# Performance work log

Measured on AMD Instinct MI355X. Metric: run time of the kernel, lower is better.

## Reference

```python
import jax, jax.numpy as jnp
import numpy as np
import math

RCR = 5.2
NUM_SPECIES = 7
AEV_DIM = 1008
WIDTHS = [1008, 256, 192, 160]


def setup_inputs() -> dict:
    key = jax.random.key(0)
    ks = jax.random.split(key, 12)
    B, N = 1, 2048
    species = jax.random.randint(ks[0], (B, N), 0, NUM_SPECIES, dtype=jnp.int64 if jax.config.read('jax_enable_x64') else jnp.int32)
    coordinates = jax.random.uniform(ks[1], (B, N, 3), dtype=jnp.float32) * 6.0
    EtaR = jnp.array([16.0], dtype=jnp.float32)
    ShfR = jnp.array([0.9 + 0.18 * x for x in range(16)], dtype=jnp.float32)
    s = 0.05
    W0 = jax.random.normal(ks[2], (NUM_SPECIES, WIDTHS[1], WIDTHS[0]), jnp.float32) * s
    b0 = jax.random.normal(ks[3], (NUM_SPECIES, WIDTHS[1]), jnp.float32) * s
    W1 = jax.random.normal(ks[4], (NUM_SPECIES, WIDTHS[2], WIDTHS[1]), jnp.float32) * s
    b1 = jax.random.normal(ks[5], (NUM_SPECIES, WIDTHS[2]), jnp.float32) * s
    W2 = jax.random.normal(ks[6], (NUM_SPECIES, WIDTHS[3], WIDTHS[2]), jnp.float32) * s
    b2 = jax.random.normal(ks[7], (NUM_SPECIES, WIDTHS[3]), jnp.float32) * s
    Wf = jax.random.normal(ks[8], (NUM_SPECIES, 1, WIDTHS[3]), jnp.float32) * s
    bf = jax.random.normal(ks[9], (NUM_SPECIES, 1), jnp.float32) * s
    return {'species': species, 'coordinates': coordinates, 'EtaR': EtaR, 'ShfR': ShfR,
            'W0': W0, 'b0': b0, 'W1': W1, 'b1': b1, 'W2': W2, 'b2': b2, 'Wf': Wf, 'bf': bf}


def _celu(x, alpha=0.1):
    return jnp.maximum(x, 0.0) + jnp.minimum(0.0, alpha * jnp.expm1(x / alpha))


def _aev(species, coordinates, EtaR, ShfR):
    B, N = species.shape
    diff = coordinates[:, :, None, :] - coordinates[:, None, :, :]  # [B,N,N,3]
    dsq = jnp.sum(diff * diff, axis=-1)
    safe = jnp.where(dsq > 0, dsq, 1.0)
    dist = jnp.sqrt(safe)  # [B,N,N], diag is a dummy 1.0
    mask = (dsq > 0) & (dist <= RCR)
    fc = (0.5 * jnp.cos(math.pi * dist / RCR) + 0.5) * mask.astype(jnp.float32)
    onehot = jax.nn.one_hot(species, NUM_SPECIES, dtype=jnp.float32)  # [B,N,S]
    core = jnp.exp(-EtaR[0] * (dist[..., None] - ShfR) ** 2)  # [B,N,N,R]
    weighted = core * fc[..., None]
    # sum over neighbor j, grouped by neighbor species s (species-major concat order)
    radial = jnp.einsum('bijr,bjs->bisr', weighted, onehot)  # [B,N,S,R]
    radial = radial.reshape(B, N, NUM_SPECIES * ShfR.shape[0])
    pad = AEV_DIM - radial.shape[-1]
    return jnp.pad(radial, ((0, 0), (0, 0), (0, pad)))


def reference(species, coordinates, EtaR, ShfR, W0, b0, W1, b1, W2, b2, Wf, bf):
    aev = _aev(species, coordinates, EtaR, ShfR)  # [B,N,1008]
    # run all 7 element nets on every atom (matches the module's redundant-compute semantics)
    h = _celu(jnp.einsum('soh,bnh->sbno', W0, aev) + b0[:, None, None, :])
    h = _celu(jnp.einsum('soh,sbnh->sbno', W1, h) + b1[:, None, None, :])
    h = _celu(jnp.einsum('soh,sbnh->sbno', W2, h) + b2[:, None, None, :])
    e = jnp.einsum('soh,sbnh->sbno', Wf, h) + bf[:, None, None, :]  # [S,B,N,1]
    onehot = jax.nn.one_hot(species, NUM_SPECIES, dtype=jnp.float32)  # [B,N,S]
    total = jnp.einsum('sbn,bns->', e[..., 0], onehot)
    return total.reshape(1)
```

## Files before the change

kernel.cpp:

```cpp
#include <hip/hip_runtime.h>

#define N_ATOMS 2048
#define NSPEC 7
#define NR 16
#define NFEAT 112
#define K0P 128
#define RCR_F 5.2f
#define H0 256
#define H1 192
#define H2 160
#define W0_PITCH 1008
#define NTILE16 128
#define GY2 (H2 / 16)
#define NPART (NSPEC * GY2 * NTILE16)

typedef __attribute__((ext_vector_type(8))) short short8;
typedef __attribute__((ext_vector_type(4))) float floatx4;

#define WS_SEG     0
#define WS_SCOORD  16384
#define WS_AEVB    65536
#define WS_H0B     655360
#define WS_H1B     1769472
#define WS_WB0     2621440
#define WS_WB1     3145728
#define WS_WB2     3866624
#define WS_PART    4325376

__device__ __forceinline__ float celu01(float x) {
    return x > 0.f ? x : 0.1f * (__expf(x * 10.f) - 1.f);
}

__device__ __forceinline__ unsigned short f2bf(float x) {
    unsigned int u = __float_as_uint(x);
    u = (u + 0x7FFFu + ((u >> 16) & 1u)) >> 16;
    return (unsigned short)u;
}

__global__ __launch_bounds__(256) void sort_kernel(const int* __restrict__ species,
                                                   const float* __restrict__ coords,
                                                   int* __restrict__ seg,
                                                   float4* __restrict__ scoord,
                                                   float* __restrict__ out) {
    __shared__ int cnt[NSPEC];
    __shared__ int cur[NSPEC];
    int t = threadIdx.x;
    if (t < NSPEC) cnt[t] = 0;
    __syncthreads();
    for (int a = t; a < N_ATOMS; a += 256) atomicAdd(&cnt[species[a]], 1);
    __syncthreads();
    if (t == 0) {
        int run = 0;
        for (int s = 0; s < NSPEC; s++) { seg[s] = run; cur[s] = run; run += cnt[s]; }
        seg[NSPEC] = run;
        out[0] = 0.0f;
    }
    __syncthreads();
    for (int a = t; a < N_ATOMS; a += 256) {
        int sp = species[a];
        int pos = atomicAdd(&cur[sp], 1);
        scoord[pos] = make_float4(coords[3*a], coords[3*a+1], coords[3*a+2], 0.f);
    }
}

#define S0E (NSPEC * H0 * K0P)
#define S1E (NSPEC * H1 * H0)
#define S2E (NSPEC * H2 * H1)
__global__ __launch_bounds__(256) void prep_kernel(const float* __restrict__ W0,
                                                   const float* __restrict__ W1,
                                                   const float* __restrict__ W2,
                                                   unsigned short* __restrict__ wb0,
                                                   unsigned short* __restrict__ wb1,
                                                   unsigned short* __restrict__ wb2) {
    int idx = blockIdx.x * 256 + threadIdx.x;
    if (idx < S0E) {
        int k = idx & 127, r = idx >> 7;
        float v = (k < NFEAT) ? W0[(size_t)r * W0_PITCH + k] : 0.f;
        wb0[idx] = f2bf(v);
    } else if (idx < S0E + S1E) {
        int j = idx - S0E;
        wb1[j] = f2bf(W1[j]);
    } else if (idx < S0E + S1E + S2E) {
        int j = idx - S0E - S1E;
        wb2[j] = f2bf(W2[j]);
    }
}

__global__ __launch_bounds__(256) void aev_kernel(const float4* __restrict__ scoord,
                                                  const int* __restrict__ seg,
                                                  const float* __restrict__ ShfR,
                                                  const float* __restrict__ EtaR,
                                                  unsigned short* __restrict__ aevb) {
    int s = blockIdx.y;
    int p = blockIdx.x * 4 + (threadIdx.x >> 6);
    int lane = threadIdx.x & 63;

    float4 ci = scoord[p];
    float eta = EtaR[0];
    float shf[NR];
#pragma unroll
    for (int r = 0; r < NR; r++) shf[r] = ShfR[r];
    float acc[NR];
#pragma unroll
    for (int r = 0; r < NR; r++) acc[r] = 0.f;

    int kbeg = seg[s] + lane;
    int kend = seg[s + 1];
    const float rc2 = RCR_F * RCR_F;
    const float cosk = 3.14159265358979f / RCR_F;

    for (int k = kbeg; k < kend; k += 64) {
        float4 cj = scoord[k];
        float dx = ci.x - cj.x, dy = ci.y - cj.y, dz = ci.z - cj.z;
        float dsq = dx*dx + dy*dy + dz*dz;
        bool valid = (dsq > 0.f) && (dsq <= rc2);
        float d = sqrtf(dsq);
        float fc = 0.5f * __cosf(d * cosk) + 0.5f;
        fc = valid ? fc : 0.f;
#pragma unroll
        for (int r = 0; r < NR; r++) {
            float u = d - shf[r];
            acc[r] = fmaf(__expf(-eta * u * u), fc, acc[r]);
        }
    }
#pragma unroll
    for (int r = 0; r < NR; r++) {
        float v = acc[r];
        v += __shfl_xor(v, 1);
        v += __shfl_xor(v, 2);
        v += __shfl_xor(v, 4);
        v += __shfl_xor(v, 8);
        v += __shfl_xor(v, 16);
        v += __shfl_xor(v, 32);
        acc[r] = v;
    }
    if (lane == 0) {
        unsigned short* dst = aevb + (size_t)p * K0P + s * NR;
#pragma unroll
        for (int r = 0; r < NR; r++) dst[r] = f2bf(acc[r]);
        if (s == 0) {
            unsigned short* pz = aevb + (size_t)p * K0P + NFEAT;
#pragma unroll
            for (int r = 0; r < K0P - NFEAT; r++) pz[r] = 0;
        }
    }
}

template<int KSTEPS, int KP, int NTOT, int NPOUT>
__global__ __launch_bounds__(64) void mfma_layer(const unsigned short* __restrict__ act,
                                                 const unsigned short* __restrict__ wb,
                                                 const float* __restrict__ bias,
                                                 const int* __restrict__ seg,
                                                 unsigned short* __restrict__ outbuf) {
    int s = blockIdx.z;
    int segend = seg[s + 1];
    int base = seg[s] + blockIdx.x * 16;
    if (base >= segend) return;
    int nbase = blockIdx.y * 16;

    int lane = threadIdx.x;
    int r = lane & 15, quad = lane >> 4;

    const unsigned short* arow = act + (size_t)(base + r) * KP + quad * 8;
    const unsigned short* brow = wb + ((size_t)(s * NTOT + nbase + r)) * KP + quad * 8;

    floatx4 acc = {0.f, 0.f, 0.f, 0.f};
#pragma unroll
    for (int ks = 0; ks < KSTEPS; ks++) {
        short8 a = *(const short8*)(arow + ks * 32);
        short8 b = *(const short8*)(brow + ks * 32);
        acc = __builtin_amdgcn_mfma_f32_16x16x32_bf16(a, b, acc, 0, 0, 0);
    }
    float bi = bias[s * NTOT + nbase + r];
#pragma unroll
    for (int reg = 0; reg < 4; reg++) {
        int atom = base + quad * 4 + reg;
        if (atom < segend)
            outbuf[(size_t)atom * NPOUT + nbase + r] = f2bf(celu01(acc[reg] + bi));
    }
}

__global__ __launch_bounds__(64) void mfma_final(const unsigned short* __restrict__ act,
                                                 const unsigned short* __restrict__ wb,
                                                 const float* __restrict__ bias,
                                                 const float* __restrict__ Wf,
                                                 const int* __restrict__ seg,
                                                 float* __restrict__ part) {
    int s = blockIdx.z;
    int pidx = (s * GY2 + blockIdx.y) * NTILE16 + blockIdx.x;
    int segend = seg[s + 1];
    int base = seg[s] + blockIdx.x * 16;
    int lane = threadIdx.x;
    if (base >= segend) {
        if (lane == 0) part[pidx] = 0.f;
        return;
    }
    int nbase = blockIdx.y * 16;
    int r = lane & 15, quad = lane >> 4;

    const unsigned short* arow = act + (size_t)(base + r) * H1 + quad * 8;
    const unsigned short* brow = wb + ((size_t)(s * H2 + nbase + r)) * H1 + quad * 8;

    floatx4 acc = {0.f, 0.f, 0.f, 0.f};
#pragma unroll
    for (int ks = 0; ks < H1 / 32; ks++) {
        short8 a = *(const short8*)(arow + ks * 32);
        short8 b = *(const short8*)(brow + ks * 32);
        acc = __builtin_amdgcn_mfma_f32_16x16x32_bf16(a, b, acc, 0, 0, 0);
    }
    float bi = bias[s * H2 + nbase + r];
    float wf = Wf[s * H2 + nbase + r];
    float e = 0.f;
#pragma unroll
    for (int reg = 0; reg < 4; reg++) {
        int atom = base + quad * 4 + reg;
        if (atom < segend) e += wf * celu01(acc[reg] + bi);
    }
    e += __shfl_xor(e, 1);
    e += __shfl_xor(e, 2);
    e += __shfl_xor(e, 4);
    e += __shfl_xor(e, 8);
    e += __shfl_xor(e, 16);
    e += __shfl_xor(e, 32);
    if (lane == 0) part[pidx] = e;
}

__global__ __launch_bounds__(256) void reduce_kernel(const float* __restrict__ part,
                                                     const int* __restrict__ seg,
                                                     const float* __restrict__ bf,
                                                     float* __restrict__ out) {
    __shared__ float wsum[4];
    int t = threadIdx.x;
    float v = 0.f;
    for (int i = t; i < NPART; i += 256) v += part[i];
    v += __shfl_down(v, 32);
    v += __shfl_down(v, 16);
    v += __shfl_down(v, 8);
    v += __shfl_down(v, 4);
    v += __shfl_down(v, 2);
    v += __shfl_down(v, 1);
    if ((t & 63) == 0) wsum[t >> 6] = v;
    __syncthreads();
    if (t == 0) {
        float tot = wsum[0] + wsum[1] + wsum[2] + wsum[3];
        for (int s = 0; s < NSPEC; s++) tot += (float)(seg[s + 1] - seg[s]) * bf[s];
        out[0] = tot;
    }
}

extern "C" void kernel_launch(void* const* d_in, const int* in_sizes, int n_in,
                              void* d_out, int out_size, void* d_ws, size_t ws_size,
                              hipStream_t stream) {
    const int*   species = (const int*)d_in[0];
    const float* coords  = (const float*)d_in[1];
    const float* EtaR    = (const float*)d_in[2];
    const float* ShfR    = (const float*)d_in[3];
    const float* W0      = (const float*)d_in[4];
    const float* b0      = (const float*)d_in[5];
    const float* W1      = (const float*)d_in[6];
    const float* b1      = (const float*)d_in[7];
    const float* W2      = (const float*)d_in[8];
    const float* b2      = (const float*)d_in[9];
    const float* Wf      = (const float*)d_in[10];
    const float* bf      = (const float*)d_in[11];
    float* out = (float*)d_out;
    char* ws = (char*)d_ws;

    int*            seg    = (int*)(ws + WS_SEG);
    float4*         scoord = (float4*)(ws + WS_SCOORD);
    unsigned short* aevb   = (unsigned short*)(ws + WS_AEVB);
    unsigned short* h0b    = (unsigned short*)(ws + WS_H0B);
    unsigned short* h1b    = (unsigned short*)(ws + WS_H1B);
    unsigned short* wb0    = (unsigned short*)(ws + WS_WB0);
    unsigned short* wb1    = (unsigned short*)(ws + WS_WB1);
    unsigned short* wb2    = (unsigned short*)(ws + WS_WB2);
    float*          part   = (float*)(ws + WS_PART);

    hipLaunchKernelGGL(sort_kernel, dim3(1), dim3(256), 0, stream,
                       species, coords, seg, scoord, out);
    hipLaunchKernelGGL(prep_kernel, dim3((S0E + S1E + S2E + 255) / 256), dim3(256), 0, stream,
                       W0, W1, W2, wb0, wb1, wb2);
    hipLaunchKernelGGL(aev_kernel, dim3(N_ATOMS / 4, NSPEC), dim3(256), 0, stream,
                       scoord, seg, ShfR, EtaR, aevb);
    hipLaunchKernelGGL((mfma_layer<K0P / 32, K0P, H0, H0>), dim3(NTILE16, H0 / 16, NSPEC),
                       dim3(64), 0, stream, aevb, wb0, b0, seg, h0b);
    hipLaunchKernelGGL((mfma_layer<H0 / 32, H0, H1, H1>), dim3(NTILE16, H1 / 16, NSPEC),
                       dim3(64), 0, stream, h0b, wb1, b1, seg, h1b);
    hipLaunchKernelGGL(mfma_final, dim3(NTILE16, GY2, NSPEC), dim3(64), 0, stream,
                       h1b, wb2, b2, Wf, seg, part);
    hipLaunchKernelGGL(reduce_kernel, dim3(1), dim3(256), 0, stream,
                       part, seg, bf, out);
}
```

Before: 157.3 us.

## Fuse MLP layers into one kernel with LDS activations and atomic reduction

The three per-layer MFMA kernels and the final reduce kernel are replaced by one kernel per 16-atom tile. It keeps the AEV tile and the hidden activations in shared memory, computes all output tiles across four waves, and accumulates the energy with atomicAdd into the output. The sort and weight-prep kernels are also merged into one launch. This removes global round trips for the hidden activations and several kernel launches. In exchange, weights are re-read per atom tile, and the atomic float adds make the summation order nondeterministic.

```diff
diff --git a/kernel.cpp b/kernel.cpp
--- a/kernel.cpp
+++ b/kernel.cpp
@@ -10,9 +10,8 @@
 #define H1 192
 #define H2 160
 #define W0_PITCH 1008
-#define NTILE16 128
-#define GY2 (H2 / 16)
-#define NPART (NSPEC * GY2 * NTILE16)
+#define MT 16
+#define NTILE16 (N_ATOMS / MT)
 
 typedef __attribute__((ext_vector_type(8))) short short8;
 typedef __attribute__((ext_vector_type(4))) float floatx4;
@@ -20,12 +19,14 @@
 #define WS_SEG     0
 #define WS_SCOORD  16384
 #define WS_AEVB    65536
-#define WS_H0B     655360
-#define WS_H1B     1769472
 #define WS_WB0     2621440
 #define WS_WB1     3145728
 #define WS_WB2     3866624
-#define WS_PART    4325376
+
+#define S0E (NSPEC * H0 * K0P)
+#define S1E (NSPEC * H1 * H0)
+#define S2E (NSPEC * H2 * H1)
+#define PREP_TOT (S0E + S1E + S2E)
 
 __device__ __forceinline__ float celu01(float x) {
     return x > 0.f ? x : 0.1f * (__expf(x * 10.f) - 1.f);
@@ -37,52 +38,48 @@
     return (unsigned short)u;
 }
 
-__global__ __launch_bounds__(256) void sort_kernel(const int* __restrict__ species,
-                                                   const float* __restrict__ coords,
-                                                   int* __restrict__ seg,
-                                                   float4* __restrict__ scoord,
-                                                   float* __restrict__ out) {
-    __shared__ int cnt[NSPEC];
-    __shared__ int cur[NSPEC];
+__global__ __launch_bounds__(256) void setup_kernel(const int* __restrict__ species,
+                                                    const float* __restrict__ coords,
+                                                    const float* __restrict__ W0,
+                                                    const float* __restrict__ W1,
+                                                    const float* __restrict__ W2,
+                                                    int* __restrict__ seg,
+                                                    float4* __restrict__ scoord,
+                                                    unsigned short* __restrict__ wb0,
+                                                    unsigned short* __restrict__ wb1,
+                                                    unsigned short* __restrict__ wb2,
+                                                    float* __restrict__ out) {
     int t = threadIdx.x;
-    if (t < NSPEC) cnt[t] = 0;
-    __syncthreads();
-    for (int a = t; a < N_ATOMS; a += 256) atomicAdd(&cnt[species[a]], 1);
-    __syncthreads();
-    if (t == 0) {
-        int run = 0;
-        for (int s = 0; s < NSPEC; s++) { seg[s] = run; cur[s] = run; run += cnt[s]; }
-        seg[NSPEC] = run;
-        out[0] = 0.0f;
-    }
-    __syncthreads();
-    for (int a = t; a < N_ATOMS; a += 256) {
-        int sp = species[a];
-        int pos = atomicAdd(&cur[sp], 1);
-        scoord[pos] = make_float4(coords[3*a], coords[3*a+1], coords[3*a+2], 0.f);
-    }
-}
-
-#define S0E (NSPEC * H0 * K0P)
-#define S1E (NSPEC * H1 * H0)
-#define S2E (NSPEC * H2 * H1)
-__global__ __launch_bounds__(256) void prep_kernel(const float* __restrict__ W0,
-                                                   const float* __restrict__ W1,
-                                                   const float* __restrict__ W2,
-                                                   unsigned short* __restrict__ wb0,
-                                                   unsigned short* __restrict__ wb1,
-                                                   unsigned short* __restrict__ wb2) {
-    int idx = blockIdx.x * 256 + threadIdx.x;
-    if (idx < S0E) {
-        int k = idx & 127, r = idx >> 7;
-        float v = (k < NFEAT) ? W0[(size_t)r * W0_PITCH + k] : 0.f;
-        wb0[idx] = f2bf(v);
-    } else if (idx < S0E + S1E) {
-        int j = idx - S0E;
-        wb1[j] = f2bf(W1[j]);
-    } else if (idx < S0E + S1E + S2E) {
-        int j = idx - S0E - S1E;
-        wb2[j] = f2bf(W2[j]);
+    if (blockIdx.x == 0) {
+        __shared__ int cnt[NSPEC];
+        __shared__ int cur[NSPEC];
+        if (t < NSPEC) cnt[t] = 0;
+        __syncthreads();
+        for (int a = t; a < N_ATOMS; a += 256) atomicAdd(&cnt[species[a]], 1);
+        __syncthreads();
+        if (t == 0) {
+            int run = 0;
+            for (int s = 0; s < NSPEC; s++) { seg[s] = run; cur[s] = run; run += cnt[s]; }
+            seg[NSPEC] = run;
+            out[0] = 0.0f;
+        }
+        __syncthreads();
+        for (int a = t; a < N_ATOMS; a += 256) {
+            int sp = species[a];
+            int pos = atomicAdd(&cur[sp], 1);
+            scoord[pos] = make_float4(coords[3*a], coords[3*a+1], coords[3*a+2], 0.f);
+        }
+    } else {
+        int idx = (blockIdx.x - 1) * 256 + t;
+        if (idx < S0E) {
+            int k = idx & 127, r = idx >> 7;
+            float v = (k < NFEAT) ? W0[(size_t)r * W0_PITCH + k] : 0.f;
+            wb0[idx] = f2bf(v);
+        } else if (idx < S0E + S1E) {
+            wb1[idx - S0E] = f2bf(W1[idx - S0E]);
+        } else {
+            wb2[idx - S0E - S1E] = f2bf(W2[idx - S0E - S1E]);
+        }
     }
 }
 
@@ -146,106 +143,105 @@
     }
 }
 
-template<int KSTEPS, int KP, int NTOT, int NPOUT>
-__global__ __launch_bounds__(64) void mfma_layer(const unsigned short* __restrict__ act,
-                                                 const unsigned short* __restrict__ wb,
-                                                 const float* __restrict__ bias,
+__global__ __launch_bounds__(256) void mlp_fused(const unsigned short* __restrict__ aevb,
+                                                 const unsigned short* __restrict__ wb0,
+                                                 const unsigned short* __restrict__ wb1,
+                                                 const unsigned short* __restrict__ wb2,
+                                                 const float* __restrict__ b0,
+                                                 const float* __restrict__ b1,
+                                                 const float* __restrict__ b2,
+                                                 const float* __restrict__ Wf,
+                                                 const float* __restrict__ bf,
                                                  const int* __restrict__ seg,
-                                                 unsigned short* __restrict__ outbuf) {
-    int s = blockIdx.z;
+                                                 float* __restrict__ out) {
+    __shared__ unsigned short aevs[MT][K0P + 8];
+    __shared__ unsigned short h0s[MT][H0 + 8];
+    __shared__ unsigned short h1s[MT][H1 + 8];
+
+    int s = blockIdx.z * 0 + blockIdx.y;
     int segend = seg[s + 1];
-    int base = seg[s] + blockIdx.x * 16;
+    int base = seg[s] + blockIdx.x * MT;
     if (base >= segend) return;
-    int nbase = blockIdx.y * 16;
-
-    int lane = threadIdx.x;
+    int n_act = min(MT, segend - base);
+
+    int t = threadIdx.x;
+    int w = t >> 6, lane = t & 63;
     int r = lane & 15, quad = lane >> 4;
 
-    const unsigned short* arow = act + (size_t)(base + r) * KP + quad * 8;
-    const unsigned short* brow = wb + ((size_t)(s * NTOT + nbase + r)) * KP + quad * 8;
-
-    floatx4 acc = {0.f, 0.f, 0.f, 0.f};
-#pragma unroll
-    for (int ks = 0; ks < KSTEPS; ks++) {
-        short8 a = *(const short8*)(arow + ks * 32);
-        short8 b = *(const short8*)(brow + ks * 32);
-        acc = __builtin_amdgcn_mfma_f32_16x16x32_bf16(a, b, acc, 0, 0, 0);
-    }
-    float bi = bias[s * NTOT + nbase + r];
-#pragma unroll
-    for (int reg = 0; reg < 4; reg++) {
-        int atom = base + quad * 4 + reg;
-        if (atom < segend)
-            outbuf[(size_t)atom * NPOUT + nbase + r] = f2bf(celu01(acc[reg] + bi));
-    }
-}
-
-__global__ __launch_bounds__(64) void mfma_final(const unsigned short* __restrict__ act,
-                                                 const unsigned short* __restrict__ wb,
-                                                 const float* __restrict__ bias,
-                                                 const float* __restrict__ Wf,
-                                                 const int* __restrict__ seg,
-                                                 float* __restrict__ part) {
-    int s = blockIdx.z;
-    int pidx = (s * GY2 + blockIdx.y) * NTILE16 + blockIdx.x;
-    int segend = seg[s + 1];
-    int base = seg[s] + blockIdx.x * 16;
-    int lane = threadIdx.x;
-    if (base >= segend) {
-        if (lane == 0) part[pidx] = 0.f;
-        return;
-    }
-    int nbase = blockIdx.y * 16;
-    int r = lane & 15, quad = lane >> 4;
-
-    const unsigned short* arow = act + (size_t)(base + r) * H1 + quad * 8;
-    const unsigned short* brow = wb + ((size_t)(s * H2 + nbase + r)) * H1 + quad * 8;
-
-    floatx4 acc = {0.f, 0.f, 0.f, 0.f};
-#pragma unroll
-    for (int ks = 0; ks < H1 / 32; ks++) {
-        short8 a = *(const short8*)(arow + ks * 32);
-        short8 b = *(const short8*)(brow + ks * 32);
-        acc = __builtin_amdgcn_mfma_f32_16x16x32_bf16(a, b, acc, 0, 0, 0);
-    }
-    float bi = bias[s * H2 + nbase + r];
-    float wf = Wf[s * H2 + nbase + r];
+    {
+        int row = t >> 4, chunk = t & 15;
+        const short8* src = (const short8*)(aevb + (size_t)(base + row) * K0P + chunk * 8);
+        *(short8*)&aevs[row][chunk * 8] = *src;
+    }
+    __syncthreads();
+
+#pragma unroll
+    for (int it = 0; it < 4; it++) {
+        int nbase = (it * 4 + w) * 16;
+        const unsigned short* brow = wb0 + ((size_t)(s * H0 + nbase + r)) * K0P + quad * 8;
+        floatx4 acc = {0.f, 0.f, 0.f, 0.f};
+#pragma unroll
+        for (int ks = 0; ks < K0P / 32; ks++) {
+            short8 a = *(const short8*)&aevs[r][ks * 32 + quad * 8];
+            short8 b = *(const short8*)(brow + ks * 32);
+            acc = __builtin_amdgcn_mfma_f32_16x16x32_bf16(a, b, acc, 0, 0, 0);
+        }
+        float bi = b0[s * H0 + nbase + r];
+#pragma unroll
+        for (int reg = 0; reg < 4; reg++)
+            h0s[quad * 4 + reg][nbase + r] = f2bf(celu01(acc[reg] + bi));
+    }
+    __syncthreads();
+
+#pragma unroll
+    for (int it = 0; it < 3; it++) {
+        int nbase = (it * 4 + w) * 16;
+        const unsigned short* brow = wb1 + ((size_t)(s * H1 + nbase + r)) * H0 + quad * 8;
+        floatx4 acc = {0.f, 0.f, 0.f, 0.f};
+#pragma unroll
+        for (int ks = 0; ks < H0 / 32; ks++) {
+            short8 a = *(const short8*)&h0s[r][ks * 32 + quad * 8];
+            short8 b = *(const short8*)(brow + ks * 32);
+            acc = __builtin_amdgcn_mfma_f32_16x16x32_bf16(a, b, acc, 0, 0, 0);
+        }
+        float bi = b1[s * H1 + nbase + r];
+#pragma unroll
+        for (int reg = 0; reg < 4; reg++)
+            h1s[quad * 4 + reg][nbase + r] = f2bf(celu01(acc[reg] + bi));
+    }
+    __syncthreads();
+
     float e = 0.f;
 #pragma unroll
-    for (int reg = 0; reg < 4; reg++) {
-        int atom = base + quad * 4 + reg;
-        if (atom < segend) e += wf * celu01(acc[reg] + bi);
-    }
+    for (int it = 0; it < 3; it++) {
+        int nt = it * 4 + w;
+        if (nt >= H2 / 16) break;
+        int nbase = nt * 16;
+        const unsigned short* brow = wb2 + ((size_t)(s * H2 + nbase + r)) * H1 + quad * 8;
+        floatx4 acc = {0.f, 0.f, 0.f, 0.f};
+#pragma unroll
+        for (int ks = 0; ks < H1 / 32; ks++) {
+            short8 a = *(const short8*)&h1s[r][ks * 32 + quad * 8];
+            short8 b = *(const short8*)(brow + ks * 32);
+            acc = __builtin_amdgcn_mfma_f32_16x16x32_bf16(a, b, acc, 0, 0, 0);
+        }
+        float bi = b2[s * H2 + nbase + r];
+        float wf = Wf[s * H2 + nbase + r];
+#pragma unroll
+        for (int reg = 0; reg < 4; reg++) {
+            int atom = base + quad * 4 + reg;
+            if (atom < segend) e += wf * celu01(acc[reg] + bi);
+        }
+    }
+    if (t == 0) e += (float)n_act * bf[s];
+
     e += __shfl_xor(e, 1);
     e += __shfl_xor(e, 2);
     e += __shfl_xor(e, 4);
     e += __shfl_xor(e, 8);
     e += __shfl_xor(e, 16);
     e += __shfl_xor(e, 32);
-    if (lane == 0) part[pidx] = e;
-}
-
-__global__ __launch_bounds__(256) void reduce_kernel(const float* __restrict__ part,
-                                                     const int* __restrict__ seg,
-                                                     const float* __restrict__ bf,
-                                                     float* __restrict__ out) {
-    __shared__ float wsum[4];
-    int t = threadIdx.x;
-    float v = 0.f;
-    for (int i = t; i < NPART; i += 256) v += part[i];
-    v += __shfl_down(v, 32);
-    v += __shfl_down(v, 16);
-    v += __shfl_down(v, 8);
-    v += __shfl_down(v, 4);
-    v += __shfl_down(v, 2);
-    v += __shfl_down(v, 1);
-    if ((t & 63) == 0) wsum[t >> 6] = v;
-    __syncthreads();
-    if (t == 0) {
-        float tot = wsum[0] + wsum[1] + wsum[2] + wsum[3];
-        for (int s = 0; s < NSPEC; s++) tot += (float)(seg[s + 1] - seg[s]) * bf[s];
-        out[0] = tot;
-    }
+    if (lane == 0) atomicAdd(out, e);
 }
 
 extern "C" void kernel_launch(void* const* d_in, const int* in_sizes, int n_in,
@@ -269,25 +265,14 @@
     int*            seg    = (int*)(ws + WS_SEG);
     float4*         scoord = (float4*)(ws + WS_SCOORD);
     unsigned short* aevb   = (unsigned short*)(ws + WS_AEVB);
-    unsigned short* h0b    = (unsigned short*)(ws + WS_H0B);
-    unsigned short* h1b    = (unsigned short*)(ws + WS_H1B);
     unsigned short* wb0    = (unsigned short*)(ws + WS_WB0);
     unsigned short* wb1    = (unsigned short*)(ws + WS_WB1);
     unsigned short* wb2    = (unsigned short*)(ws + WS_WB2);
-    float*          part   = (float*)(ws + WS_PART);
-
-    hipLaunchKernelGGL(sort_kernel, dim3(1), dim3(256), 0, stream,
-                       species, coords, seg, scoord, out);
-    hipLaunchKernelGGL(prep_kernel, dim3((S0E + S1E + S2E + 255) / 256), dim3(256), 0, stream,
-                       W0, W1, W2, wb0, wb1, wb2);
+
+    hipLaunchKernelGGL(setup_kernel, dim3(1 + PREP_TOT / 256), dim3(256), 0, stream,
+                       species, coords, W0, W1, W2, seg, scoord, wb0, wb1, wb2, out);
     hipLaunchKernelGGL(aev_kernel, dim3(N_ATOMS / 4, NSPEC), dim3(256), 0, stream,
                        scoord, seg, ShfR, EtaR, aevb);
-    hipLaunchKernelGGL((mfma_layer<K0P / 32, K0P, H0, H0>), dim3(NTILE16, H0 / 16, NSPEC),
-                       dim3(64), 0, stream, aevb, wb0, b0, seg, h0b);
-    hipLaunchKernelGGL((mfma_layer<H0 / 32, H0, H1, H1>), dim3(NTILE16, H1 / 16, NSPEC),
-                       dim3(64), 0, stream, h0b, wb1, b1, seg, h1b);
-    hipLaunchKernelGGL(mfma_final, dim3(NTILE16, GY2, NSPEC), dim3(64), 0, stream,
-                       h1b, wb2, b2, Wf, seg, part);
-    hipLaunchKernelGGL(reduce_kernel, dim3(1), dim3(256), 0, stream,
-                       part, seg, bf, out);
-}
+    hipLaunchKernelGGL(mlp_fused, dim3(NTILE16, NSPEC), dim3(256), 0, stream,
+                       aevb, wb0, wb1, wb2, b0, b1, b2, Wf, bf, seg, out);
+}
```

Result: faster. 133.9 us (-14.9%).
